# Optimization experiments

Hardware: AMD Instinct MI355X
Metric: run time of the kernel (lower is better)

The kernel has to match this reference:

```python
import jax, jax.numpy as jnp
import numpy as np

B, L, K, D = 1024, 8, 16, 64
_KSCALE = 1.0 / np.sqrt(K * D)  # keep channel roughly norm-preserving over layers


def setup_inputs() -> dict:
    key = jax.random.key(0)
    k1, k2, k3, k4 = jax.random.split(key, 4)
    state_re = jax.random.normal(k1, (B, D, D), dtype=jnp.float32)
    state_im = jax.random.normal(k2, (B, D, D), dtype=jnp.float32)
    kraus_re = jax.random.normal(k3, (L, K, D, D), dtype=jnp.float32) * _KSCALE
    kraus_im = jax.random.normal(k4, (L, K, D, D), dtype=jnp.float32) * _KSCALE
    return {"state_re": state_re, "state_im": state_im,
            "kraus_re": kraus_re, "kraus_im": kraus_im}


def reference(state_re, state_im, kraus_re, kraus_im):
    # rho: [B, d, d] complex density matrices; kraus: [L, K, d, d]
    rho = (state_re + 1j * state_im).astype(jnp.complex64)
    kraus = (kraus_re + 1j * kraus_im).astype(jnp.complex64)

    def layer_step(rho, Kl):
        # Kl: [K, d, d]. output_state = sum_k  K_k @ rho @ K_k^dagger
        tmp = jnp.einsum('kij,bjl->kbil', Kl, rho)            # K_k @ rho
        rho_new = jnp.einsum('kbil,kml->bim', tmp, Kl.conj())  # (...) @ K_k^dagger, summed over k
        return rho_new, None

    rho, _ = jax.lax.scan(layer_step, rho, kraus)
    # return real/imag stacked as float32: [2, B, d, d]
    return jnp.stack([rho.real, rho.imag])
```

## Files before the change

### kernel.cpp

```cpp
#include <hip/hip_runtime.h>
#include <hip/hip_fp16.h>

#define D 64
#define NKR 16
#define NB 1024
#define NL 8

typedef __attribute__((ext_vector_type(8))) _Float16 half8;
typedef __attribute__((ext_vector_type(16))) float f32x16;
typedef __attribute__((ext_vector_type(4))) int i32x4;

static __device__ __forceinline__ half8 neg8(half8 x) {
    i32x4 u = __builtin_bit_cast(i32x4, x);
    u = u ^ (int)0x80008000;
    return __builtin_bit_cast(half8, u);
}

union Pack4 { _Float16 h[4]; uint2 u; };

#define GLDS16(gp, lp) \
    __builtin_amdgcn_global_load_lds((const __attribute__((address_space(1))) void*)(gp), \
                                     (__attribute__((address_space(3))) void*)(lp), 16, 0, 0)

__global__ void kconv_kernel(const float* __restrict__ re, const float* __restrict__ im,
                             _Float16* __restrict__ out) {
    int plane = blockIdx.y;
    int idx = blockIdx.x * blockDim.x + threadIdx.x;
    const float* src = plane ? im : re;
    float4 v = ((const float4*)src)[idx];
    int e = idx * 4;
    int lk = e >> 12;
    int rem = e & 4095;
    int row = rem >> 6, col = rem & 63;
    int grp = (col >> 3) ^ (row & 7);
    Pack4 p;
    p.h[0] = (_Float16)v.x; p.h[1] = (_Float16)v.y;
    p.h[2] = (_Float16)v.z; p.h[3] = (_Float16)v.w;
    *(uint2*)(out + ((size_t)lk * 2 + plane) * 4096 + row * 64 + grp * 8 + (col & 7)) = p.u;
}

__global__ void sconv_kernel(const float* __restrict__ re, const float* __restrict__ im,
                             _Float16* __restrict__ out) {
    __shared__ float tile[64][65];
    int b = blockIdx.x;
    int t = threadIdx.x;
    for (int plane = 0; plane < 2; ++plane) {
        const float* src = (plane ? im : re) + (size_t)b * 4096;
        __syncthreads();
        #pragma unroll
        for (int i = 0; i < 16; ++i) {
            int e = t + 256 * i;
            tile[e >> 6][e & 63] = src[e];
        }
        __syncthreads();
        _Float16* o = out + ((size_t)b * 2 + plane) * 4096;
        #pragma unroll
        for (int i = 0; i < 16; ++i) {
            int e = t + 256 * i;
            o[e] = (_Float16)tile[e & 63][e >> 6];
        }
    }
}

__global__ __launch_bounds__(256, 2) void layer_kernel(
    const _Float16* __restrict__ rho_in,
    _Float16* __restrict__ rho_out,
    float* __restrict__ final_out,
    const _Float16* __restrict__ kraus,
    int last)
{
    __shared__ __align__(16) _Float16 Klds[2 * D * D];
    __shared__ __align__(16) _Float16 Trow[2][2][D * D];

    const int b0   = blockIdx.x * 2;
    const int t    = threadIdx.x;
    const int wv   = t >> 6;
    const int lane = t & 63;
    const int l31  = lane & 31;
    const int hl   = lane >> 5;
    const int wr   = wv >> 1;
    const int wc   = wv & 1;

    half8 a1re[2][4], a1im[2][4];
    #pragma unroll
    for (int r = 0; r < 2; ++r) {
        const _Float16* rb = rho_in + (size_t)(b0 + r) * 2 * D * D;
        const int row = 32 * wr + l31;
        #pragma unroll
        for (int ks = 0; ks < 4; ++ks) {
            const int col = 16 * ks + 8 * hl;
            a1re[r][ks] = *(const half8*)(rb + row * D + col);
            a1im[r][ks] = *(const half8*)(rb + D * D + row * D + col);
        }
    }

    {
        const char* kb = (const char*)kraus;
        const int off = wv * 4096;
        #pragma unroll
        for (int rr = 0; rr < 4; ++rr)
            GLDS16(kb + off + rr * 1024 + lane * 16, (char*)Klds + off + rr * 1024);
    }

    f32x16 accRe[2], accIm[2];
    #pragma unroll
    for (int r = 0; r < 2; ++r)
        #pragma unroll
        for (int i = 0; i < 16; ++i) { accRe[r][i] = 0.f; accIm[r][i] = 0.f; }

    __syncthreads();

    const int row1 = 32 * wc + l31;
    const int rb1  = row1 * 64;
    const int rx1  = row1 & 7;
    const int iS1  = 32 * wc + l31;
    const int x1   = iS1 & 7;
    const int iS2  = 32 * wr + l31;
    const int x2   = iS2 & 7;

    #pragma unroll 1
    for (int k = 0; k < NKR; ++k) {
        half8 bre[4], bim[4], bimn[4];
        #pragma unroll
        for (int ks = 0; ks < 4; ++ks) {
            const int g = ((2 * ks + hl) ^ rx1) * 8;
            bre[ks]  = *(const half8*)&Klds[rb1 + g];
            bim[ks]  = *(const half8*)&Klds[4096 + rb1 + g];
            bimn[ks] = neg8(bim[ks]);
        }

        #pragma unroll
        for (int r = 0; r < 2; ++r) {
            f32x16 dd;
            #pragma unroll
            for (int i = 0; i < 16; ++i) dd[i] = 0.f;
            #pragma unroll
            for (int ks = 0; ks < 4; ++ks) {
                dd = __builtin_amdgcn_mfma_f32_32x32x16_f16(a1re[r][ks], bre[ks],  dd, 0, 0, 0);
                dd = __builtin_amdgcn_mfma_f32_32x32x16_f16(a1im[r][ks], bimn[ks], dd, 0, 0, 0);
            }
            #pragma unroll
            for (int g = 0; g < 4; ++g) {
                Pack4 pr;
                #pragma unroll
                for (int j = 0; j < 4; ++j) pr.h[j] = (_Float16)dd[4 * g + j];
                *(uint2*)&Trow[r][0][iS1 * 64 + (((4 * wr + g) ^ x1) * 8) + 4 * hl] = pr.u;
            }
            #pragma unroll
            for (int i = 0; i < 16; ++i) dd[i] = 0.f;
            #pragma unroll
            for (int ks = 0; ks < 4; ++ks) {
                dd = __builtin_amdgcn_mfma_f32_32x32x16_f16(a1re[r][ks], bim[ks], dd, 0, 0, 0);
                dd = __builtin_amdgcn_mfma_f32_32x32x16_f16(a1im[r][ks], bre[ks], dd, 0, 0, 0);
            }
            #pragma unroll
            for (int g = 0; g < 4; ++g) {
                Pack4 pi;
                #pragma unroll
                for (int j = 0; j < 4; ++j) pi.h[j] = (_Float16)dd[4 * g + j];
                *(uint2*)&Trow[r][1][iS1 * 64 + (((4 * wr + g) ^ x1) * 8) + 4 * hl] = pi.u;
            }
        }
        __syncthreads();

        if (k + 1 < NKR) {
            const char* kb = (const char*)(kraus + (size_t)(k + 1) * 2 * D * D);
            const int off = wv * 4096;
            #pragma unroll
            for (int rr = 0; rr < 4; ++rr)
                GLDS16(kb + off + rr * 1024 + lane * 16, (char*)Klds + off + rr * 1024);
        }

        #pragma unroll
        for (int ks = 0; ks < 4; ++ks) {
            const int lcol = 16 * ks + 8 * hl;
            const int toff = iS2 * 64 + (((lcol >> 3) ^ x2) * 8);
            #pragma unroll
            for (int r = 0; r < 2; ++r) {
                half8 are = *(const half8*)&Trow[r][0][toff];
                half8 aim = *(const half8*)&Trow[r][1][toff];
                accRe[r] = __builtin_amdgcn_mfma_f32_32x32x16_f16(are, bre[ks],  accRe[r], 0, 0, 0);
                accRe[r] = __builtin_amdgcn_mfma_f32_32x32x16_f16(aim, bim[ks],  accRe[r], 0, 0, 0);
                accIm[r] = __builtin_amdgcn_mfma_f32_32x32x16_f16(aim, bre[ks],  accIm[r], 0, 0, 0);
                accIm[r] = __builtin_amdgcn_mfma_f32_32x32x16_f16(are, bimn[ks], accIm[r], 0, 0, 0);
            }
        }
        __syncthreads();
    }

    const int m = 32 * wc + l31;
    if (!last) {
        #pragma unroll
        for (int r = 0; r < 2; ++r) {
            _Float16* ob = rho_out + (size_t)(b0 + r) * 2 * D * D;
            #pragma unroll
            for (int g = 0; g < 4; ++g) {
                Pack4 pr, pi;
                #pragma unroll
                for (int j = 0; j < 4; ++j) {
                    pr.h[j] = (_Float16)accRe[r][4 * g + j];
                    pi.h[j] = (_Float16)accIm[r][4 * g + j];
                }
                const int i0 = 32 * wr + 8 * g + 4 * hl;
                *(uint2*)(ob + m * D + i0)         = pr.u;
                *(uint2*)(ob + D * D + m * D + i0) = pi.u;
            }
        }
    } else {
        #pragma unroll
        for (int r = 0; r < 2; ++r) {
            float* o0 = final_out + (size_t)(b0 + r) * 4096;
            float* o1 = final_out + (size_t)(NB + b0 + r) * 4096;
            #pragma unroll
            for (int g = 0; g < 4; ++g) {
                #pragma unroll
                for (int j = 0; j < 4; ++j) {
                    const int i = 32 * wr + 8 * g + 4 * hl + j;
                    o0[i * D + m] = accRe[r][4 * g + j];
                    o1[i * D + m] = accIm[r][4 * g + j];
                }
            }
        }
    }
}

extern "C" void kernel_launch(void* const* d_in, const int* in_sizes, int n_in,
                              void* d_out, int out_size, void* d_ws, size_t ws_size,
                              hipStream_t stream) {
    const float* state_re = (const float*)d_in[0];
    const float* state_im = (const float*)d_in[1];
    const float* kraus_re = (const float*)d_in[2];
    const float* kraus_im = (const float*)d_in[3];

    _Float16* kraus_h = (_Float16*)d_ws;
    _Float16* bufA = (_Float16*)d_out;
    _Float16* bufB = (_Float16*)((char*)d_out + (size_t)NB * 2 * D * D * sizeof(_Float16));
    float* fout = (float*)d_out;

    kconv_kernel<<<dim3(512, 2), 256, 0, stream>>>(kraus_re, kraus_im, kraus_h);
    sconv_kernel<<<NB, 256, 0, stream>>>(state_re, state_im, bufA);

    for (int l = 0; l < NL; ++l) {
        const _Float16* in = (l & 1) ? bufB : bufA;
        _Float16* out      = (l & 1) ? bufA : bufB;
        layer_kernel<<<NB / 2, 256, 0, stream>>>(in, out, fout,
                                                 kraus_h + (size_t)l * NKR * 2 * D * D,
                                                 (l == NL - 1) ? 1 : 0);
    }
}
```

Before: 568.9 us.

## Keep intermediate K@rho in registers via permlane swap, double-buffer Kraus LDS

Reassigns work so each wave pair owns one batch matrix and computes both row halves. The first product's accumulator tiles are repacked into MFMA A-operand fragments in registers with v_permlane32_swap instead of a round trip through the Trow LDS buffer. Kraus operators are now double-buffered in LDS with a 4-element XOR swizzle, which removes one __syncthreads per Kraus step. The cost is extra MFMA work, since each wave now computes the full intermediate for its batch, plus more register pressure and more LDS reads of the Kraus rows.

```diff
diff --git a/kernel.cpp b/kernel.cpp
--- a/kernel.cpp
+++ b/kernel.cpp
@@ -16,11 +16,23 @@
     return __builtin_bit_cast(half8, u);
 }
 
+static __device__ __forceinline__ unsigned pkrtz(float a, float b) {
+    auto h = __builtin_amdgcn_cvt_pkrtz(a, b);
+    return __builtin_bit_cast(unsigned, h);
+}
+
+static __device__ __forceinline__ void plswap(unsigned &a, unsigned &b) {
+    asm volatile("v_permlane32_swap_b32 %0, %1" : "+v"(a), "+v"(b));
+}
+
 union Pack4 { _Float16 h[4]; uint2 u; };
+union H8 { unsigned u[4]; uint2 v[2]; half8 h; };
 
 #define GLDS16(gp, lp) \
     __builtin_amdgcn_global_load_lds((const __attribute__((address_space(1))) void*)(gp), \
                                      (__attribute__((address_space(3))) void*)(lp), 16, 0, 0)
+
+#define MFMA __builtin_amdgcn_mfma_f32_32x32x16_f16
 
 __global__ void kconv_kernel(const float* __restrict__ re, const float* __restrict__ im,
                              _Float16* __restrict__ out) {
@@ -32,11 +44,11 @@
     int lk = e >> 12;
     int rem = e & 4095;
     int row = rem >> 6, col = rem & 63;
-    int grp = (col >> 3) ^ (row & 7);
+    int grp = (col >> 2) ^ (row & 15);
     Pack4 p;
     p.h[0] = (_Float16)v.x; p.h[1] = (_Float16)v.y;
     p.h[2] = (_Float16)v.z; p.h[3] = (_Float16)v.w;
-    *(uint2*)(out + ((size_t)lk * 2 + plane) * 4096 + row * 64 + grp * 8 + (col & 7)) = p.u;
+    *(uint2*)(out + ((size_t)lk * 2 + plane) * 4096 + row * 64 + grp * 4) = p.u;
 }
 
 __global__ void sconv_kernel(const float* __restrict__ re, const float* __restrict__ im,
@@ -62,6 +74,98 @@
     }
 }
 
+static __device__ __forceinline__ void exchange(const f32x16 &dd, half8 &f0, half8 &f1) {
+    unsigned A0 = pkrtz(dd[0],  dd[1]),  B0 = pkrtz(dd[2],  dd[3]);
+    unsigned A1 = pkrtz(dd[4],  dd[5]),  B1 = pkrtz(dd[6],  dd[7]);
+    unsigned A2 = pkrtz(dd[8],  dd[9]),  B2 = pkrtz(dd[10], dd[11]);
+    unsigned A3 = pkrtz(dd[12], dd[13]), B3 = pkrtz(dd[14], dd[15]);
+    plswap(A0, A1);
+    plswap(B0, B1);
+    plswap(A2, A3);
+    plswap(B2, B3);
+    H8 h0; h0.u[0] = A0; h0.u[1] = B0; h0.u[2] = A1; h0.u[3] = B1; f0 = h0.h;
+    H8 h1; h1.u[0] = A2; h1.u[1] = B2; h1.u[2] = A3; h1.u[3] = B3; f1 = h1.h;
+}
+
+template<int IT>
+static __device__ __forceinline__ void kstep(
+    const _Float16* __restrict__ KB,
+    const half8 (&a1re)[2][4], const half8 (&a1im)[2][4],
+    f32x16 (&accRe)[2], f32x16 (&accIm)[2],
+    int l31, int hl)
+{
+    half8 bre0[4], bim0[4];
+    {
+        const int brow = 32 * IT + l31;
+        const int base = brow * 64;
+        const int rx = brow & 15;
+        #pragma unroll
+        for (int ks = 0; ks < 4; ++ks) {
+            const int g = 4 * ks + 2 * hl;
+            const int p = ((g ^ rx) << 2);
+            const int q = (((g + 1) ^ rx) << 2);
+            H8 t;
+            t.v[0] = *(const uint2*)&KB[base + p];
+            t.v[1] = *(const uint2*)&KB[base + q];
+            bre0[ks] = t.h;
+            t.v[0] = *(const uint2*)&KB[4096 + base + p];
+            t.v[1] = *(const uint2*)&KB[4096 + base + q];
+            bim0[ks] = t.h;
+        }
+    }
+
+    half8 af_re[4], af_im[4];
+    #pragma unroll
+    for (int lh = 0; lh < 2; ++lh) {
+        f32x16 ddre, ddim;
+        #pragma unroll
+        for (int i = 0; i < 16; ++i) { ddre[i] = 0.f; ddim[i] = 0.f; }
+        #pragma unroll
+        for (int ks = 0; ks < 4; ++ks) {
+            half8 bn = neg8(bim0[ks]);
+            ddre = MFMA(a1re[lh][ks], bre0[ks], ddre, 0, 0, 0);
+            ddre = MFMA(a1im[lh][ks], bn,       ddre, 0, 0, 0);
+            ddim = MFMA(a1re[lh][ks], bim0[ks], ddim, 0, 0, 0);
+            ddim = MFMA(a1im[lh][ks], bre0[ks], ddim, 0, 0, 0);
+        }
+        exchange(ddre, af_re[2 * lh], af_re[2 * lh + 1]);
+        exchange(ddim, af_im[2 * lh], af_im[2 * lh + 1]);
+    }
+
+    #pragma unroll
+    for (int ks = 0; ks < 4; ++ks) {
+        half8 an = neg8(af_re[ks]);
+        accRe[IT] = MFMA(af_re[ks], bre0[ks], accRe[IT], 0, 0, 0);
+        accRe[IT] = MFMA(af_im[ks], bim0[ks], accRe[IT], 0, 0, 0);
+        accIm[IT] = MFMA(af_im[ks], bre0[ks], accIm[IT], 0, 0, 0);
+        accIm[IT] = MFMA(an,        bim0[ks], accIm[IT], 0, 0, 0);
+    }
+
+    {
+        const int brow = 32 * (1 - IT) + l31;
+        const int base = brow * 64;
+        const int rx = brow & 15;
+        #pragma unroll
+        for (int ks = 0; ks < 4; ++ks) {
+            const int g = 4 * ks + 2 * hl;
+            const int p = ((g ^ rx) << 2);
+            const int q = (((g + 1) ^ rx) << 2);
+            H8 t;
+            t.v[0] = *(const uint2*)&KB[base + p];
+            t.v[1] = *(const uint2*)&KB[base + q];
+            half8 br = t.h;
+            t.v[0] = *(const uint2*)&KB[4096 + base + p];
+            t.v[1] = *(const uint2*)&KB[4096 + base + q];
+            half8 bi = t.h;
+            half8 an = neg8(af_re[ks]);
+            accRe[1 - IT] = MFMA(af_re[ks], br, accRe[1 - IT], 0, 0, 0);
+            accRe[1 - IT] = MFMA(af_im[ks], bi, accRe[1 - IT], 0, 0, 0);
+            accIm[1 - IT] = MFMA(af_im[ks], br, accIm[1 - IT], 0, 0, 0);
+            accIm[1 - IT] = MFMA(an,        bi, accIm[1 - IT], 0, 0, 0);
+        }
+    }
+}
+
 __global__ __launch_bounds__(256, 2) void layer_kernel(
     const _Float16* __restrict__ rho_in,
     _Float16* __restrict__ rho_out,
@@ -69,8 +173,7 @@
     const _Float16* __restrict__ kraus,
     int last)
 {
-    __shared__ __align__(16) _Float16 Klds[2 * D * D];
-    __shared__ __align__(16) _Float16 Trow[2][2][D * D];
+    __shared__ __align__(16) _Float16 Klds[2][2 * D * D];
 
     const int b0   = blockIdx.x * 2;
     const int t    = threadIdx.x;
@@ -82,15 +185,17 @@
     const int wc   = wv & 1;
 
     half8 a1re[2][4], a1im[2][4];
-    #pragma unroll
-    for (int r = 0; r < 2; ++r) {
-        const _Float16* rb = rho_in + (size_t)(b0 + r) * 2 * D * D;
-        const int row = 32 * wr + l31;
-        #pragma unroll
-        for (int ks = 0; ks < 4; ++ks) {
-            const int col = 16 * ks + 8 * hl;
-            a1re[r][ks] = *(const half8*)(rb + row * D + col);
-            a1im[r][ks] = *(const half8*)(rb + D * D + row * D + col);
+    {
+        const _Float16* rb = rho_in + (size_t)(b0 + wc) * 2 * D * D;
+        #pragma unroll
+        for (int lh = 0; lh < 2; ++lh) {
+            const int row = 32 * lh + l31;
+            #pragma unroll
+            for (int ks = 0; ks < 4; ++ks) {
+                const int col = 16 * ks + 8 * hl;
+                a1re[lh][ks] = *(const half8*)(rb + row * D + col);
+                a1im[lh][ks] = *(const half8*)(rb + D * D + row * D + col);
+            }
         }
     }
 
@@ -99,107 +204,45 @@
         const int off = wv * 4096;
         #pragma unroll
         for (int rr = 0; rr < 4; ++rr)
-            GLDS16(kb + off + rr * 1024 + lane * 16, (char*)Klds + off + rr * 1024);
+            GLDS16(kb + off + rr * 1024 + lane * 16, (char*)&Klds[0][0] + off + rr * 1024);
     }
 
     f32x16 accRe[2], accIm[2];
     #pragma unroll
-    for (int r = 0; r < 2; ++r)
-        #pragma unroll
-        for (int i = 0; i < 16; ++i) { accRe[r][i] = 0.f; accIm[r][i] = 0.f; }
+    for (int mt = 0; mt < 2; ++mt)
+        #pragma unroll
+        for (int i = 0; i < 16; ++i) { accRe[mt][i] = 0.f; accIm[mt][i] = 0.f; }
 
     __syncthreads();
-
-    const int row1 = 32 * wc + l31;
-    const int rb1  = row1 * 64;
-    const int rx1  = row1 & 7;
-    const int iS1  = 32 * wc + l31;
-    const int x1   = iS1 & 7;
-    const int iS2  = 32 * wr + l31;
-    const int x2   = iS2 & 7;
 
     #pragma unroll 1
     for (int k = 0; k < NKR; ++k) {
-        half8 bre[4], bim[4], bimn[4];
-        #pragma unroll
-        for (int ks = 0; ks < 4; ++ks) {
-            const int g = ((2 * ks + hl) ^ rx1) * 8;
-            bre[ks]  = *(const half8*)&Klds[rb1 + g];
-            bim[ks]  = *(const half8*)&Klds[4096 + rb1 + g];
-            bimn[ks] = neg8(bim[ks]);
-        }
-
-        #pragma unroll
-        for (int r = 0; r < 2; ++r) {
-            f32x16 dd;
-            #pragma unroll
-            for (int i = 0; i < 16; ++i) dd[i] = 0.f;
-            #pragma unroll
-            for (int ks = 0; ks < 4; ++ks) {
-                dd = __builtin_amdgcn_mfma_f32_32x32x16_f16(a1re[r][ks], bre[ks],  dd, 0, 0, 0);
-                dd = __builtin_amdgcn_mfma_f32_32x32x16_f16(a1im[r][ks], bimn[ks], dd, 0, 0, 0);
-            }
-            #pragma unroll
-            for (int g = 0; g < 4; ++g) {
-                Pack4 pr;
-                #pragma unroll
-                for (int j = 0; j < 4; ++j) pr.h[j] = (_Float16)dd[4 * g + j];
-                *(uint2*)&Trow[r][0][iS1 * 64 + (((4 * wr + g) ^ x1) * 8) + 4 * hl] = pr.u;
-            }
-            #pragma unroll
-            for (int i = 0; i < 16; ++i) dd[i] = 0.f;
-            #pragma unroll
-            for (int ks = 0; ks < 4; ++ks) {
-                dd = __builtin_amdgcn_mfma_f32_32x32x16_f16(a1re[r][ks], bim[ks], dd, 0, 0, 0);
-                dd = __builtin_amdgcn_mfma_f32_32x32x16_f16(a1im[r][ks], bre[ks], dd, 0, 0, 0);
-            }
-            #pragma unroll
-            for (int g = 0; g < 4; ++g) {
-                Pack4 pi;
-                #pragma unroll
-                for (int j = 0; j < 4; ++j) pi.h[j] = (_Float16)dd[4 * g + j];
-                *(uint2*)&Trow[r][1][iS1 * 64 + (((4 * wr + g) ^ x1) * 8) + 4 * hl] = pi.u;
-            }
-        }
-        __syncthreads();
-
         if (k + 1 < NKR) {
             const char* kb = (const char*)(kraus + (size_t)(k + 1) * 2 * D * D);
             const int off = wv * 4096;
             #pragma unroll
             for (int rr = 0; rr < 4; ++rr)
-                GLDS16(kb + off + rr * 1024 + lane * 16, (char*)Klds + off + rr * 1024);
-        }
-
-        #pragma unroll
-        for (int ks = 0; ks < 4; ++ks) {
-            const int lcol = 16 * ks + 8 * hl;
-            const int toff = iS2 * 64 + (((lcol >> 3) ^ x2) * 8);
-            #pragma unroll
-            for (int r = 0; r < 2; ++r) {
-                half8 are = *(const half8*)&Trow[r][0][toff];
-                half8 aim = *(const half8*)&Trow[r][1][toff];
-                accRe[r] = __builtin_amdgcn_mfma_f32_32x32x16_f16(are, bre[ks],  accRe[r], 0, 0, 0);
-                accRe[r] = __builtin_amdgcn_mfma_f32_32x32x16_f16(aim, bim[ks],  accRe[r], 0, 0, 0);
-                accIm[r] = __builtin_amdgcn_mfma_f32_32x32x16_f16(aim, bre[ks],  accIm[r], 0, 0, 0);
-                accIm[r] = __builtin_amdgcn_mfma_f32_32x32x16_f16(are, bimn[ks], accIm[r], 0, 0, 0);
-            }
-        }
+                GLDS16(kb + off + rr * 1024 + lane * 16,
+                       (char*)&Klds[(k + 1) & 1][0] + off + rr * 1024);
+        }
+        const _Float16* KB = &Klds[0][0] + (k & 1) * (2 * D * D);
+        if (wr == 0) kstep<0>(KB, a1re, a1im, accRe, accIm, l31, hl);
+        else         kstep<1>(KB, a1re, a1im, accRe, accIm, l31, hl);
         __syncthreads();
     }
 
-    const int m = 32 * wc + l31;
     if (!last) {
-        #pragma unroll
-        for (int r = 0; r < 2; ++r) {
-            _Float16* ob = rho_out + (size_t)(b0 + r) * 2 * D * D;
+        _Float16* ob = rho_out + (size_t)(b0 + wc) * 2 * D * D;
+        #pragma unroll
+        for (int mt = 0; mt < 2; ++mt) {
+            const int m = 32 * mt + l31;
             #pragma unroll
             for (int g = 0; g < 4; ++g) {
                 Pack4 pr, pi;
                 #pragma unroll
                 for (int j = 0; j < 4; ++j) {
-                    pr.h[j] = (_Float16)accRe[r][4 * g + j];
-                    pi.h[j] = (_Float16)accIm[r][4 * g + j];
+                    pr.h[j] = (_Float16)accRe[mt][4 * g + j];
+                    pi.h[j] = (_Float16)accIm[mt][4 * g + j];
                 }
                 const int i0 = 32 * wr + 8 * g + 4 * hl;
                 *(uint2*)(ob + m * D + i0)         = pr.u;
@@ -207,17 +250,18 @@
             }
         }
     } else {
-        #pragma unroll
-        for (int r = 0; r < 2; ++r) {
-            float* o0 = final_out + (size_t)(b0 + r) * 4096;
-            float* o1 = final_out + (size_t)(NB + b0 + r) * 4096;
+        float* o0 = final_out + (size_t)(b0 + wc) * 4096;
+        float* o1 = final_out + (size_t)(NB + b0 + wc) * 4096;
+        #pragma unroll
+        for (int mt = 0; mt < 2; ++mt) {
+            const int m = 32 * mt + l31;
             #pragma unroll
             for (int g = 0; g < 4; ++g) {
                 #pragma unroll
                 for (int j = 0; j < 4; ++j) {
                     const int i = 32 * wr + 8 * g + 4 * hl + j;
-                    o0[i * D + m] = accRe[r][4 * g + j];
-                    o1[i * D + m] = accIm[r][4 * g + j];
+                    o0[i * D + m] = accRe[mt][4 * g + j];
+                    o1[i * D + m] = accIm[mt][4 * g + j];
                 }
             }
         }
```

Measured after the change: 570.4 us. Within noise of the previous version (+0.3%).
